# Performance work log

Hardware: AMD Instinct MI355X
Metric: run time of the kernel (lower is better)

The kernel has to match this reference:

```python
import jax, jax.numpy as jnp
import numpy as np

TAU = 2.0       # init_tau
VTH = 1.0       # v_threshold
VRESET = 0.0    # v_reset (hard reset)
ALPHA = 2.0     # ATan surrogate width
H = 8           # num_heads
W = 20          # attention_window
TIME_STEP = 2   # config.time_step -> global_scale uses 1000 // time_step


@jax.custom_vjp
def spike(x):
    return (x >= 0.0).astype(x.dtype)

def _spike_fwd(x):
    return (x >= 0.0).astype(x.dtype), x

def _spike_bwd(x, g):
    # ATan surrogate gradient (spikingjelly default)
    sg = (ALPHA / 2.0) / (1.0 + (jnp.pi / 2.0 * ALPHA * x) ** 2)
    return (g * sg,)

spike.defvjp(_spike_fwd, _spike_bwd)


def lif(x_seq):
    """Multi-step LIF, decay_input=False, hard reset. x_seq: [T, ...] -> spikes [T, ...]."""
    def step(v, x):
        h = v - (v - VRESET) / TAU + x          # neuronal charge (decay_input=False)
        s = spike(h - VTH)
        v_new = s * VRESET + (1.0 - s) * h      # hard reset
        return v_new, s
    _, s_seq = jax.lax.scan(step, jnp.zeros_like(x_seq[0]), x_seq)
    return s_seq


def bn(x, gamma, beta, eps=1e-5):
    # BatchNorm1d step_mode='m': stats over (T, B) per channel (training-mode stats)
    mean = x.mean(axis=(0, 1))
    var = x.var(axis=(0, 1))
    return (x - mean) * jax.lax.rsqrt(var + eps) * gamma + beta


def _shift(a, o):
    # a: [B, H, T, D]; out[..., t, :] = a[..., t + o, :], zero outside -> local band
    if o == 0:
        return a
    B_, H_, T_, D_ = a.shape
    z = jnp.zeros((B_, H_, abs(o), D_), a.dtype)
    if o > 0:
        return jnp.concatenate([a[:, :, o:, :], z], axis=2)
    return jnp.concatenate([z, a[:, :, :o, :]], axis=2)


def _forward(x, wq, wk, wv, w_mattn, w_proj, w_dw, w_pw, bn_gamma, bn_beta):
    T, B, C = x.shape
    D = C // H
    local_scale = 1.0 / np.sqrt(D * (2 * W + 1)).astype(np.float32)
    global_scale = 1.0 / np.sqrt(D * (1000 // TIME_STEP)).astype(np.float32)

    # spiking QKV: pointwise conv (kernel 1) + BN + LIF
    q = lif(bn(jnp.einsum('tbc,dc->tbd', x, wq), bn_gamma[0], bn_beta[0]))
    k = lif(bn(jnp.einsum('tbc,dc->tbd', x, wk), bn_gamma[1], bn_beta[1]))
    v = lif(bn(jnp.einsum('tbc,dc->tbd', x, wv), bn_gamma[2], bn_beta[2]))

    heads = lambda a: a.reshape(T, B, H, D).transpose(1, 2, 0, 3)   # [B,H,T,D]
    unheads = lambda a: a.transpose(2, 0, 1, 3).reshape(T, B, C)    # [T,B,C]
    qh, kh, vh = heads(q), heads(k), heads(v)

    # global spiking self-attention (no softmax): (Q K^T) V * global_scale
    attn = jnp.einsum('bhtd,bhsd->bhts', qh, kh)
    g_spk = lif(unheads(jnp.einsum('bhts,bhsd->bhtd', attn, vh) * global_scale))

    # local sliding-window attention over offsets [-W, W] (banded, no [T,T] matrix)
    out_l = jnp.zeros_like(vh)
    for o in range(-W, W + 1):
        s = jnp.einsum('bhtd,bhtd->bht', qh, _shift(kh, o))
        out_l = out_l + s[..., None] * _shift(vh, o)
    l_spk = lif(unheads(out_l * local_scale))

    # depthwise temporal conv branch on V: v_dw -> LIF -> v_pw (1x1 over heads)
    dw = jax.lax.conv_general_dilated(
        vh, w_dw, window_strides=(1, 1), padding=((4, 4), (0, 0)),
        dimension_numbers=('NCHW', 'OIHW', 'NCHW'), feature_group_count=H)
    dw_spk_h = heads(lif(unheads(dw)))
    dw_out = unheads(jnp.einsum('bhtd,gh->bgtd', dw_spk_h, w_pw))

    # merge branches, then mattn conv+BN+LIF and proj conv+BN+LIF
    y0 = lif(g_spk + l_spk + dw_out)
    y1 = lif(bn(jnp.einsum('tbc,dc->tbd', y0, w_mattn), bn_gamma[3], bn_beta[3]))
    out = lif(bn(jnp.einsum('tbc,dc->tbd', y1, w_proj), bn_gamma[4], bn_beta[4]))
    return out


def setup_inputs() -> dict:
    key = jax.random.key(0)
    ks = jax.random.split(key, 10)
    T, B, C = 500, 8, 512
    sc = 0.03
    x = jax.random.normal(ks[0], (T, B, C), jnp.float32)
    wq = jax.random.normal(ks[1], (C, C), jnp.float32) * sc
    wk = jax.random.normal(ks[2], (C, C), jnp.float32) * sc
    wv = jax.random.normal(ks[3], (C, C), jnp.float32) * sc
    w_mattn = jax.random.normal(ks[4], (C, C), jnp.float32) * sc
    w_proj = jax.random.normal(ks[5], (C, C), jnp.float32) * sc
    w_dw = jax.random.normal(ks[6], (H, 1, 9, 1), jnp.float32) * 0.3   # depthwise (9,1)
    w_pw = jax.random.normal(ks[7], (H, H), jnp.float32) * 0.3         # 1x1 over heads
    bn_gamma = jax.random.uniform(ks[8], (5, C), jnp.float32) + 0.5
    bn_beta = jax.random.normal(ks[9], (5, C), jnp.float32) * 0.1
    return {'x': x, 'wq': wq, 'wk': wk, 'wv': wv, 'w_mattn': w_mattn,
            'w_proj': w_proj, 'w_dw': w_dw, 'w_pw': w_pw,
            'bn_gamma': bn_gamma, 'bn_beta': bn_beta}


def reference(x, wq, wk, wv, w_mattn, w_proj, w_dw, w_pw, bn_gamma, bn_beta):
    return _forward(x, wq, wk, wv, w_mattn, w_proj, w_dw, w_pw, bn_gamma, bn_beta)
```

## Files before the change

### kernel.cpp

```cpp
#include <hip/hip_runtime.h>
#include <cmath>

#define TT 500
#define NTOT 2048000
#define WW 20

typedef _Float16 f16x8 __attribute__((ext_vector_type(8)));
typedef _Float16 f16x4 __attribute__((ext_vector_type(4)));
typedef float f32x4 __attribute__((ext_vector_type(4)));

#define C1SC 4.8828125e-4f
#define C2SC 2.384185791015625e-7f

__global__ __launch_bounds__(256) void prep_split_k(
    const float* __restrict__ x, const float* __restrict__ wq,
    const float* __restrict__ wk, const float* __restrict__ wv,
    const float* __restrict__ wm, const float* __restrict__ wp,
    _Float16* __restrict__ X0, _Float16* __restrict__ X1, _Float16* __restrict__ X2,
    _Float16* __restrict__ Q0, _Float16* __restrict__ Q1, _Float16* __restrict__ Q2,
    _Float16* __restrict__ M0, _Float16* __restrict__ M1, _Float16* __restrict__ M2,
    _Float16* __restrict__ P0, _Float16* __restrict__ P1, _Float16* __restrict__ P2)
{
    int gid = blockIdx.x * 256 + threadIdx.x;
    const float* src;
    _Float16 *d0, *d1, *d2;
    size_t si, di;
    if (gid < 512000) {
        src = x; d0 = X0; d1 = X1; d2 = X2; si = di = (size_t)gid * 4;
    } else if (gid < 708608) {
        int g = gid - 512000;
        int s3 = g >> 16;
        src = (s3 == 0) ? wq : ((s3 == 1) ? wk : wv);
        d0 = Q0; d1 = Q1; d2 = Q2;
        si = (size_t)(g & 65535) * 4;
        di = (size_t)g * 4;
    } else if (gid < 774144) {
        int g = gid - 708608;
        src = wm; d0 = M0; d1 = M1; d2 = M2; si = di = (size_t)g * 4;
    } else {
        int g = gid - 774144;
        src = wp; d0 = P0; d1 = P1; d2 = P2; si = di = (size_t)g * 4;
    }
    float4 v = *(const float4*)(src + si);
    float f[4] = {v.x, v.y, v.z, v.w};
    f16x4 a, b, c;
#pragma unroll
    for (int i = 0; i < 4; ++i) {
        _Float16 h0 = (_Float16)f[i];
        float r1 = f[i] - (float)h0;
        _Float16 h1 = (_Float16)(r1 * 2048.0f);
        float r2 = r1 - (float)h1 * C1SC;
        _Float16 h2 = (_Float16)(r2 * 4194304.0f);
        a[i] = h0; b[i] = h1; c[i] = h2;
    }
    *(f16x4*)(d0 + di) = a;
    *(f16x4*)(d1 + di) = b;
    *(f16x4*)(d2 + di) = c;
}

__global__ __launch_bounds__(256) void gemm_f16s3_k(
    const _Float16* __restrict__ X0, const _Float16* __restrict__ X1,
    const _Float16* __restrict__ X2,
    const _Float16* __restrict__ B0g, const _Float16* __restrict__ B1g,
    const _Float16* __restrict__ B2g,
    float* __restrict__ out, float* __restrict__ colpart, int M)
{
    __shared__ __align__(16) _Float16 sA[23040];
    int tid = threadIdx.x;
    int bid = blockIdx.x;
    int xcd = bid & 7;
    int j = bid >> 3;
    int mblk = (xcd << 3) | (j & 7);
    int nblk = j >> 3;
    int mBase = mblk * 64;
    int nBase = nblk * 128;
    int arow = tid >> 2;
    int ak = (tid & 3) * 8;
    int wv = tid >> 6;
    int lane = tid & 63;
    int wr = wv >> 1, wc = wv & 1;
    int lg = lane >> 4, l16 = lane & 15;

    f32x4 acc0[2][4] = {}, acc1[2][4] = {}, acc2[2][4] = {};
    f16x8 pa0, pa1, pa2, pb0[2], pb1[2], pb2[2];
    f16x8 hz = {};

    auto loadT = [&](int kt) {
        int m = mBase + arow;
        if (m < M) {
            pa0 = *(const f16x8*)(X0 + (size_t)m * 512 + kt + ak);
            pa1 = *(const f16x8*)(X1 + (size_t)m * 512 + kt + ak);
            pa2 = *(const f16x8*)(X2 + (size_t)m * 512 + kt + ak);
        } else { pa0 = hz; pa1 = hz; pa2 = hz; }
#pragma unroll
        for (int l = 0; l < 2; ++l) {
            int r = nBase + arow + l * 64;
            pb0[l] = *(const f16x8*)(B0g + (size_t)r * 512 + kt + ak);
            pb1[l] = *(const f16x8*)(B1g + (size_t)r * 512 + kt + ak);
            pb2[l] = *(const f16x8*)(B2g + (size_t)r * 512 + kt + ak);
        }
    };
    loadT(0);
    for (int kt = 0; kt < 512; kt += 32) {
        __syncthreads();
        {
            int ao = arow * 40 + ak;
            *(f16x8*)&sA[ao] = pa0;
            *(f16x8*)&sA[2560 + ao] = pa1;
            *(f16x8*)&sA[5120 + ao] = pa2;
#pragma unroll
            for (int l = 0; l < 2; ++l) {
                int bo = (arow + l * 64) * 40 + ak;
                *(f16x8*)&sA[7680 + bo] = pb0[l];
                *(f16x8*)&sA[12800 + bo] = pb1[l];
                *(f16x8*)&sA[17920 + bo] = pb2[l];
            }
        }
        __syncthreads();
        if (kt + 32 < 512) loadT(kt + 32);
        f16x8 a0f[2], a1f[2], a2f[2];
#pragma unroll
        for (int i = 0; i < 2; ++i) {
            int off = (wr * 32 + i * 16 + l16) * 40 + lg * 8;
            a0f[i] = *(const f16x8*)&sA[off];
            a1f[i] = *(const f16x8*)&sA[2560 + off];
            a2f[i] = *(const f16x8*)&sA[5120 + off];
        }
#pragma unroll
        for (int jj = 0; jj < 4; ++jj) {
            int boff = (wc * 64 + jj * 16 + l16) * 40 + lg * 8;
            f16x8 b0f = *(const f16x8*)&sA[7680 + boff];
            f16x8 b1f = *(const f16x8*)&sA[12800 + boff];
            f16x8 b2f = *(const f16x8*)&sA[17920 + boff];
#pragma unroll
            for (int i = 0; i < 2; ++i) {
                acc0[i][jj] = __builtin_amdgcn_mfma_f32_16x16x32_f16(a0f[i], b0f, acc0[i][jj], 0, 0, 0);
                acc1[i][jj] = __builtin_amdgcn_mfma_f32_16x16x32_f16(a0f[i], b1f, acc1[i][jj], 0, 0, 0);
                acc1[i][jj] = __builtin_amdgcn_mfma_f32_16x16x32_f16(a1f[i], b0f, acc1[i][jj], 0, 0, 0);
                acc2[i][jj] = __builtin_amdgcn_mfma_f32_16x16x32_f16(a1f[i], b1f, acc2[i][jj], 0, 0, 0);
                acc2[i][jj] = __builtin_amdgcn_mfma_f32_16x16x32_f16(a0f[i], b2f, acc2[i][jj], 0, 0, 0);
                acc2[i][jj] = __builtin_amdgcn_mfma_f32_16x16x32_f16(a2f[i], b0f, acc2[i][jj], 0, 0, 0);
            }
        }
    }
#pragma unroll
    for (int i = 0; i < 2; ++i)
#pragma unroll
        for (int jj = 0; jj < 4; ++jj)
#pragma unroll
            for (int r = 0; r < 4; ++r)
                acc0[i][jj][r] = fmaf(C2SC, acc2[i][jj][r],
                                      fmaf(C1SC, acc1[i][jj][r], acc0[i][jj][r]));
    __syncthreads();
    float* red = (float*)sA;
#pragma unroll
    for (int jj = 0; jj < 4; ++jj) {
        float s = 0.f, q = 0.f;
#pragma unroll
        for (int i = 0; i < 2; ++i)
#pragma unroll
            for (int r = 0; r < 4; ++r) { float v = acc0[i][jj][r]; s += v; q = fmaf(v, v, q); }
        s += __shfl_xor(s, 16, 64); s += __shfl_xor(s, 32, 64);
        q += __shfl_xor(q, 16, 64); q += __shfl_xor(q, 32, 64);
        if (lane < 16) {
            int col = wc * 64 + jj * 16 + lane;
            red[(wr * 128 + col) * 2 + 0] = s;
            red[(wr * 128 + col) * 2 + 1] = q;
        }
    }
    __syncthreads();
    if (tid < 128) {
        float ss = red[tid * 2 + 0] + red[(128 + tid) * 2 + 0];
        float qq = red[tid * 2 + 1] + red[(128 + tid) * 2 + 1];
        colpart[((size_t)mblk * 1536 + nBase + tid) * 2 + 0] = ss;
        colpart[((size_t)mblk * 1536 + nBase + tid) * 2 + 1] = qq;
    }
    int wsel = nBase >> 9;
    int col0 = nBase & 511;
    float* outp = out + (size_t)wsel * NTOT;
#pragma unroll
    for (int i = 0; i < 2; ++i) {
        int m0 = mBase + wr * 32 + i * 16 + lg * 4;
#pragma unroll
        for (int jj = 0; jj < 4; ++jj) {
            int cc = col0 + wc * 64 + jj * 16 + l16;
#pragma unroll
            for (int r = 0; r < 4; ++r) {
                int m = m0 + r;
                if (m < M) outp[(size_t)m * 512 + cc] = acc0[i][jj][r];
            }
        }
    }
}

__global__ __launch_bounds__(256) void gemm_hs3_k(
    const _Float16* __restrict__ Ah,
    const _Float16* __restrict__ B0g, const _Float16* __restrict__ B1g,
    const _Float16* __restrict__ B2g,
    float* __restrict__ out, float* __restrict__ colpart, int M)
{
    __shared__ __align__(16) _Float16 sA[10240];
    int tid = threadIdx.x;
    int bid = blockIdx.x;
    int xcd = bid & 7;
    int j = bid >> 3;
    int mblk = (xcd << 3) | (j & 7);
    int nblk = j >> 3;
    int mBase = mblk * 64;
    int col0 = nblk * 64;
    int arow = tid >> 2;
    int ak = (tid & 3) * 8;
    int wv = tid >> 6;
    int lane = tid & 63;
    int wr = wv >> 1, wc = wv & 1;
    int lg = lane >> 4, l16 = lane & 15;

    f32x4 acc0[2][2] = {}, acc1[2][2] = {}, acc2[2][2] = {};
    f16x8 pa, pb0, pb1, pb2;
    f16x8 hz = {};

    auto loadT = [&](int kt) {
        int m = mBase + arow;
        pa = (m < M) ? *(const f16x8*)(Ah + (size_t)m * 512 + kt + ak) : hz;
        int r = col0 + arow;
        pb0 = *(const f16x8*)(B0g + (size_t)r * 512 + kt + ak);
        pb1 = *(const f16x8*)(B1g + (size_t)r * 512 + kt + ak);
        pb2 = *(const f16x8*)(B2g + (size_t)r * 512 + kt + ak);
    };
    loadT(0);
    for (int kt = 0; kt < 512; kt += 32) {
        __syncthreads();
        {
            int ao = arow * 40 + ak;
            *(f16x8*)&sA[ao] = pa;
            *(f16x8*)&sA[2560 + ao] = pb0;
            *(f16x8*)&sA[5120 + ao] = pb1;
            *(f16x8*)&sA[7680 + ao] = pb2;
        }
        __syncthreads();
        if (kt + 32 < 512) loadT(kt + 32);
        f16x8 af[2];
#pragma unroll
        for (int i = 0; i < 2; ++i)
            af[i] = *(const f16x8*)&sA[(wr * 32 + i * 16 + l16) * 40 + lg * 8];
#pragma unroll
        for (int jj = 0; jj < 2; ++jj) {
            int boff = (wc * 32 + jj * 16 + l16) * 40 + lg * 8;
            f16x8 b0f = *(const f16x8*)&sA[2560 + boff];
            f16x8 b1f = *(const f16x8*)&sA[5120 + boff];
            f16x8 b2f = *(const f16x8*)&sA[7680 + boff];
#pragma unroll
            for (int i = 0; i < 2; ++i) {
                acc0[i][jj] = __builtin_amdgcn_mfma_f32_16x16x32_f16(af[i], b0f, acc0[i][jj], 0, 0, 0);
                acc1[i][jj] = __builtin_amdgcn_mfma_f32_16x16x32_f16(af[i], b1f, acc1[i][jj], 0, 0, 0);
                acc2[i][jj] = __builtin_amdgcn_mfma_f32_16x16x32_f16(af[i], b2f, acc2[i][jj], 0, 0, 0);
            }
        }
    }
#pragma unroll
    for (int i = 0; i < 2; ++i)
#pragma unroll
        for (int jj = 0; jj < 2; ++jj)
#pragma unroll
            for (int r = 0; r < 4; ++r)
                acc0[i][jj][r] = fmaf(C2SC, acc2[i][jj][r],
                                      fmaf(C1SC, acc1[i][jj][r], acc0[i][jj][r]));
    __syncthreads();
    float* red = (float*)sA;
#pragma unroll
    for (int jj = 0; jj < 2; ++jj) {
        float s = 0.f, q = 0.f;
#pragma unroll
        for (int i = 0; i < 2; ++i)
#pragma unroll
            for (int r = 0; r < 4; ++r) { float v = acc0[i][jj][r]; s += v; q = fmaf(v, v, q); }
        s += __shfl_xor(s, 16, 64); s += __shfl_xor(s, 32, 64);
        q += __shfl_xor(q, 16, 64); q += __shfl_xor(q, 32, 64);
        if (lane < 16) {
            int col = wc * 32 + jj * 16 + lane;
            red[(wr * 64 + col) * 2 + 0] = s;
            red[(wr * 64 + col) * 2 + 1] = q;
        }
    }
    __syncthreads();
    if (tid < 64) {
        float ss = red[tid * 2 + 0] + red[(64 + tid) * 2 + 0];
        float qq = red[tid * 2 + 1] + red[(64 + tid) * 2 + 1];
        colpart[((size_t)mblk * 512 + col0 + tid) * 2 + 0] = ss;
        colpart[((size_t)mblk * 512 + col0 + tid) * 2 + 1] = qq;
    }
#pragma unroll
    for (int i = 0; i < 2; ++i) {
        int m0 = mBase + wr * 32 + i * 16 + lg * 4;
#pragma unroll
        for (int jj = 0; jj < 2; ++jj) {
            int cc = col0 + wc * 32 + jj * 16 + l16;
#pragma unroll
            for (int r = 0; r < 4; ++r) {
                int m = m0 + r;
                if (m < M) out[(size_t)m * 512 + cc] = acc0[i][jj][r];
            }
        }
    }
}

__global__ __launch_bounds__(256) void lif_seg_k(
    const float* __restrict__ pre, const float* __restrict__ colpart, int CT, int chunks,
    const float* __restrict__ gamma, const float* __restrict__ beta,
    float* __restrict__ outF, unsigned char* __restrict__ outB,
    _Float16* __restrict__ outH, int segLen, int warm)
{
    int gid = blockIdx.x * 256 + threadIdx.x;
    int tensor = gid >> 12;
    int bc = gid & 4095;
    int ch = (tensor << 9) | (bc & 511);
    double s = 0.0, s2 = 0.0;
    for (int k = 0; k < chunks; ++k) {
        s  += (double)colpart[((size_t)k * CT + ch) * 2 + 0];
        s2 += (double)colpart[((size_t)k * CT + ch) * 2 + 1];
    }
    double mean = s / 4000.0;
    double var = s2 / 4000.0 - mean * mean;
    double scd = (double)gamma[ch] / sqrt(var + 1e-5);
    float sc = (float)scd;
    float sh = (float)((double)beta[ch] - mean * scd);
    const float* q0 = pre + (size_t)tensor * NTOT + bc;
    float* oF = outF ? outF + (size_t)tensor * NTOT + bc : nullptr;
    unsigned char* oB = outB ? outB + (size_t)tensor * NTOT + bc : nullptr;
    _Float16* oH = outH ? outH + (size_t)tensor * NTOT + bc : nullptr;
    int t0 = blockIdx.y * segLen;
    int twarm = (t0 - warm > 0) ? (t0 - warm) : 0;
    int tend = (t0 + segLen < TT) ? (t0 + segLen) : TT;
    float v = 0.f;
    float b0[8];
#pragma unroll
    for (int j = 0; j < 8; ++j) {
        int tt = twarm + j;
        b0[j] = (tt < tend) ? q0[(size_t)tt * 4096] : 0.f;
    }
    for (int t = twarm; t < tend; t += 8) {
        float n0[8];
#pragma unroll
        for (int j = 0; j < 8; ++j) {
            int tt = t + 8 + j;
            n0[j] = (tt < tend) ? q0[(size_t)tt * 4096] : 0.f;
        }
#pragma unroll
        for (int j = 0; j < 8; ++j) {
            int tc = t + j;
            if (tc >= tend) break;
            float bnx = fmaf(b0[j], sc, sh);
            float h = fmaf(0.5f, v, bnx);
            float sp = (h >= 1.f) ? 1.f : 0.f;
            v = (h >= 1.f) ? 0.f : h;
            if (tc >= t0) {
                if (oB)      oB[(size_t)tc * 4096] = (unsigned char)sp;
                else if (oH) oH[(size_t)tc * 4096] = (_Float16)sp;
                else         oF[(size_t)tc * 4096] = sp;
            }
        }
#pragma unroll
        for (int j = 0; j < 8; ++j) b0[j] = n0[j];
    }
}

__global__ __launch_bounds__(256) void ktv_part_k(
    const unsigned char* __restrict__ kspk, const unsigned char* __restrict__ vspk,
    float* __restrict__ part)
{
    __shared__ __align__(16) float kb[16][64], vb[16][64];
    int bh = blockIdx.x;
    int seg = blockIdx.y;
    int t0p = seg * 125, t1p = t0p + 125;
    int b = bh >> 3, h = bh & 7;
    int tid = threadIdx.x;
    int d1b = (tid >> 4) * 4, d2b = (tid & 15) * 4;
    size_t cb = (size_t)b * 512 + h * 64;
    int sRow = tid >> 4;
    int sD = (tid & 15) * 4;
    float acc[4][4] = {};
    uchar4 pk, pv;
    auto preload = [&](int tt) {
        int t = tt + sRow;
        if (t < t1p) {
            pk = *(const uchar4*)(kspk + (size_t)t * 4096 + cb + sD);
            pv = *(const uchar4*)(vspk + (size_t)t * 4096 + cb + sD);
        } else {
            pk = make_uchar4(0, 0, 0, 0); pv = make_uchar4(0, 0, 0, 0);
        }
    };
    preload(t0p);
    for (int tt = t0p; tt < t1p; tt += 16) {
        __syncthreads();
        kb[sRow][sD + 0] = (float)pk.x; kb[sRow][sD + 1] = (float)pk.y;
        kb[sRow][sD + 2] = (float)pk.z; kb[sRow][sD + 3] = (float)pk.w;
        vb[sRow][sD + 0] = (float)pv.x; vb[sRow][sD + 1] = (float)pv.y;
        vb[sRow][sD + 2] = (float)pv.z; vb[sRow][sD + 3] = (float)pv.w;
        __syncthreads();
        preload(tt + 16);
#pragma unroll
        for (int tl = 0; tl < 16; ++tl) {
            float4 k4 = *(const float4*)&kb[tl][d1b];
            float4 v4 = *(const float4*)&vb[tl][d2b];
            float ka[4] = {k4.x, k4.y, k4.z, k4.w};
            float va[4] = {v4.x, v4.y, v4.z, v4.w};
#pragma unroll
            for (int i = 0; i < 4; ++i)
#pragma unroll
                for (int j = 0; j < 4; ++j)
                    acc[i][j] = fmaf(ka[i], va[j], acc[i][j]);
        }
    }
    size_t ob = ((size_t)seg * 64 + bh) * 4096;
#pragma unroll
    for (int i = 0; i < 4; ++i)
        *(float4*)(part + ob + (size_t)(d1b + i) * 64 + d2b) =
            make_float4(acc[i][0], acc[i][1], acc[i][2], acc[i][3]);
}

__global__ __launch_bounds__(256) void ktv_reduce_k(
    const float* __restrict__ part, float* __restrict__ ktv)
{
    int i4 = (blockIdx.x * 256 + threadIdx.x) * 4;
    float4 a = *(const float4*)(part + i4);
    float4 b = *(const float4*)(part + 262144 + i4);
    float4 c = *(const float4*)(part + 2 * 262144 + i4);
    float4 d = *(const float4*)(part + 3 * 262144 + i4);
    *(float4*)(ktv + i4) = make_float4(((a.x + b.x) + c.x) + d.x,
                                       ((a.y + b.y) + c.y) + d.y,
                                       ((a.z + b.z) + c.z) + d.z,
                                       ((a.w + b.w) + c.w) + d.w);
}

__global__ __launch_bounds__(256) void gapply_t_k(
    const unsigned char* __restrict__ sq, const float* __restrict__ ktv,
    float* __restrict__ gpre, float gscale)
{
    __shared__ float qs[10][512];
    int tid = threadIdx.x;
    int t0 = blockIdx.x * 10;
    int b = blockIdx.y;
    for (int i = tid; i < 1280; i += 256) {
        int t = i >> 7;
        int c4 = (i & 127) * 4;
        uchar4 u = *(const uchar4*)(sq + (size_t)(t0 + t) * 4096 + b * 512 + c4);
        qs[t][c4 + 0] = (float)u.x; qs[t][c4 + 1] = (float)u.y;
        qs[t][c4 + 2] = (float)u.z; qs[t][c4 + 3] = (float)u.w;
    }
    __syncthreads();
#pragma unroll
    for (int half = 0; half < 2; ++half) {
        int c = tid + half * 256;
        int h = c >> 6, dcol = c & 63;
        const float* kt = ktv + ((size_t)(b * 8 + h) * 64) * 64 + dcol;
        float acc[10] = {};
        for (int d1 = 0; d1 < 64; ++d1) {
            float kv = kt[(size_t)d1 * 64];
#pragma unroll
            for (int t = 0; t < 10; ++t)
                acc[t] = fmaf(qs[t][h * 64 + d1], kv, acc[t]);
        }
#pragma unroll
        for (int t = 0; t < 10; ++t)
            gpre[(size_t)(t0 + t) * 4096 + b * 512 + c] = acc[t] * gscale;
    }
}

__global__ __launch_bounds__(256) void local_k(
    const unsigned char* __restrict__ qspk, const unsigned char* __restrict__ kspk,
    const unsigned char* __restrict__ vspk, float* __restrict__ lpre, float lscale)
{
    __shared__ __align__(16) float qs[32][68];
    __shared__ __align__(16) float ks[72][68];
    __shared__ __align__(16) float vs[72][68];
    __shared__ float sm[32][72];
    int t0 = blockIdx.x * 32;
    int bh = blockIdx.y;
    int b = bh >> 3, h = bh & 7;
    int tid = threadIdx.x;
    size_t cb = (size_t)b * 512 + h * 64;

    for (int i = tid; i < 512; i += 256) {
        int r = i >> 4, d4 = (i & 15) * 4;
        int t = t0 + r;
        if (t < TT) {
            uchar4 u = *(const uchar4*)(qspk + (size_t)t * 4096 + cb + d4);
            qs[r][d4 + 0] = (float)u.x; qs[r][d4 + 1] = (float)u.y;
            qs[r][d4 + 2] = (float)u.z; qs[r][d4 + 3] = (float)u.w;
        } else {
            qs[r][d4 + 0] = 0.f; qs[r][d4 + 1] = 0.f; qs[r][d4 + 2] = 0.f; qs[r][d4 + 3] = 0.f;
        }
    }
    for (int i = tid; i < 1152; i += 256) {
        int r = i >> 4, d4 = (i & 15) * 4;
        int u_ = t0 - WW + r;
        if (u_ >= 0 && u_ < TT) {
            uchar4 uk = *(const uchar4*)(kspk + (size_t)u_ * 4096 + cb + d4);
            uchar4 uv = *(const uchar4*)(vspk + (size_t)u_ * 4096 + cb + d4);
            ks[r][d4 + 0] = (float)uk.x; ks[r][d4 + 1] = (float)uk.y;
            ks[r][d4 + 2] = (float)uk.z; ks[r][d4 + 3] = (float)uk.w;
            vs[r][d4 + 0] = (float)uv.x; vs[r][d4 + 1] = (float)uv.y;
            vs[r][d4 + 2] = (float)uv.z; vs[r][d4 + 3] = (float)uv.w;
        } else {
            ks[r][d4 + 0] = 0.f; ks[r][d4 + 1] = 0.f; ks[r][d4 + 2] = 0.f; ks[r][d4 + 3] = 0.f;
            vs[r][d4 + 0] = 0.f; vs[r][d4 + 1] = 0.f; vs[r][d4 + 2] = 0.f; vs[r][d4 + 3] = 0.f;
        }
    }
    __syncthreads();

    int tA = tid >> 3;
    int ug = tid & 7;
    float4 qreg[16];
#pragma unroll
    for (int i = 0; i < 16; ++i) qreg[i] = *(const float4*)&qs[tA][i * 4];
#pragma unroll
    for (int ui = 0; ui < 9; ++ui) {
        int u = ug + ui * 8;
        float acc = 0.f;
#pragma unroll
        for (int i = 0; i < 16; ++i) {
            float4 k4 = *(const float4*)&ks[u][i * 4];
            acc = fmaf(qreg[i].x, k4.x, acc);
            acc = fmaf(qreg[i].y, k4.y, acc);
            acc = fmaf(qreg[i].z, k4.z, acc);
            acc = fmaf(qreg[i].w, k4.w, acc);
        }
        sm[tA][u] = acc;
    }
    __syncthreads();

#pragma unroll
    for (int oi = 0; oi < 2; ++oi) {
        int idx = tid + oi * 256;
        int t = idx >> 4;
        int dg = (idx & 15) * 4;
        float4 acc = make_float4(0.f, 0.f, 0.f, 0.f);
        for (int o = 0; o < 41; ++o) {
            int u = t + o;
            float s = sm[t][u];
            float4 v4 = *(const float4*)&vs[u][dg];
            acc.x = fmaf(s, v4.x, acc.x);
            acc.y = fmaf(s, v4.y, acc.y);
            acc.z = fmaf(s, v4.z, acc.z);
            acc.w = fmaf(s, v4.w, acc.w);
        }
        int tg = t0 + t;
        if (tg < TT) {
            acc.x *= lscale; acc.y *= lscale; acc.z *= lscale; acc.w *= lscale;
            *(float4*)(lpre + (size_t)tg * 4096 + cb + dg) = acc;
        }
    }
}

__global__ __launch_bounds__(256) void branch_y0_k(
    const float* __restrict__ gpre, const float* __restrict__ lpre,
    const unsigned char* __restrict__ sv, const float* __restrict__ wdw,
    const float* __restrict__ wpw, _Float16* __restrict__ sy0,
    int segLen, int warm)
{
    int tid = threadIdx.x;
    int wave = tid >> 6, lane = tid & 63;
    int gw = blockIdx.x * 4 + wave;
    int b = gw >> 3, dg = gw & 7;
    int h = lane >> 3, dl = lane & 7;
    int c = h * 64 + dg * 8 + dl;
    int base = b * 512 + c;
    float w9[9];
#pragma unroll
    for (int j = 0; j < 9; ++j) w9[j] = wdw[h * 9 + j];
    float w8[8];
#pragma unroll
    for (int j = 0; j < 8; ++j) w8[j] = wpw[h * 8 + j];
    int t0 = blockIdx.y * segLen;
    int twarm = (t0 - warm > 0) ? (t0 - warm) : 0;
    int tend = (t0 + segLen < TT) ? (t0 + segLen) : TT;
    float vg = 0.f, vl = 0.f, vd = 0.f, vy = 0.f;
    float win[12];
#pragma unroll
    for (int i = 0; i < 12; ++i) {
        int tt = twarm - 4 + i;
        win[i] = (tt >= 0 && tt < TT) ? (float)sv[(size_t)tt * 4096 + base] : 0.f;
    }
    float pg[4], pl[4], pv[4];
    auto pref = [&](int t) {
#pragma unroll
        for (int j = 0; j < 4; ++j) {
            int tt = t + j;
            bool in = tt < tend;
            pg[j] = in ? gpre[(size_t)tt * 4096 + base] : 0.f;
            pl[j] = in ? lpre[(size_t)tt * 4096 + base] : 0.f;
            int tv = t + 8 + j;
            pv[j] = (tv < TT) ? (float)sv[(size_t)tv * 4096 + base] : 0.f;
        }
    };
    pref(twarm);
    for (int t = twarm; t < tend; t += 4) {
        float cg[4], cl[4], cv[4];
#pragma unroll
        for (int j = 0; j < 4; ++j) { cg[j] = pg[j]; cl[j] = pl[j]; cv[j] = pv[j]; }
        pref(t + 4);
#pragma unroll
        for (int j = 0; j < 4; ++j) {
            int tc = t + j;
            if (tc >= tend) break;
            float x = 0.f;
#pragma unroll
            for (int q = 0; q < 9; ++q) x = fmaf(w9[q], win[j + q], x);
            float hd = fmaf(0.5f, vd, x);
            float sd = (hd >= 1.f) ? 1.f : 0.f;
            vd = (hd >= 1.f) ? 0.f : hd;
            float hg = fmaf(0.5f, vg, cg[j]);
            float sg = (hg >= 1.f) ? 1.f : 0.f;
            vg = (hg >= 1.f) ? 0.f : hg;
            float hl = fmaf(0.5f, vl, cl[j]);
            float sl = (hl >= 1.f) ? 1.f : 0.f;
            vl = (hl >= 1.f) ? 0.f : hl;
            float mix = 0.f;
#pragma unroll
            for (int h2 = 0; h2 < 8; ++h2)
                mix = fmaf(w8[h2], __shfl(sd, h2 * 8 + dl, 64), mix);
            float xy = (sg + sl) + mix;
            float hy = fmaf(0.5f, vy, xy);
            float sy = (hy >= 1.f) ? 1.f : 0.f;
            vy = (hy >= 1.f) ? 0.f : hy;
            if (tc >= t0) sy0[(size_t)tc * 4096 + base] = (_Float16)sy;
        }
#pragma unroll
        for (int i = 0; i < 8; ++i) win[i] = win[i + 4];
#pragma unroll
        for (int i = 0; i < 4; ++i) win[8 + i] = cv[i];
    }
}

extern "C" void kernel_launch(void* const* d_in, const int* in_sizes, int n_in,
                              void* d_out, int out_size, void* d_ws, size_t ws_size,
                              hipStream_t stream)
{
    const float* x       = (const float*)d_in[0];
    const float* wq      = (const float*)d_in[1];
    const float* wk      = (const float*)d_in[2];
    const float* wv      = (const float*)d_in[3];
    const float* w_mattn = (const float*)d_in[4];
    const float* w_proj  = (const float*)d_in[5];
    const float* w_dw    = (const float*)d_in[6];
    const float* w_pw    = (const float*)d_in[7];
    const float* bn_g    = (const float*)d_in[8];
    const float* bn_b    = (const float*)d_in[9];
    float* out = (float*)d_out;
    float* ws = (float*)d_ws;

    float gs32 = (float)std::sqrt((double)(64 * 500));
    float gscale = (float)(1.0 / (double)gs32);
    float ls32 = (float)std::sqrt((double)(64 * 41));
    float lscale = (float)(1.0 / (double)ls32);
    const int M = TT * 8;

    float* S0 = ws;
    float* S1 = ws + (size_t)NTOT;
    float* S2 = ws + 2 * (size_t)NTOT;
    float* part4   = ws + 3 * (size_t)NTOT;
    float* ktvBuf  = part4 + 4 * 262144;
    float* colpart = ktvBuf + 262144;
    unsigned char* spk = (unsigned char*)(colpart + 196608);
    unsigned char* sq  = spk;
    unsigned char* sk  = spk + (size_t)NTOT;
    unsigned char* sv  = spk + 2 * (size_t)NTOT;
    _Float16* sy0h = (_Float16*)(spk + 3 * (size_t)NTOT);
    _Float16* sy1h = (_Float16*)spk;
    _Float16* X0 = (_Float16*)spk;
    _Float16* X1 = X0 + (size_t)NTOT;
    _Float16* X2 = X1 + (size_t)NTOT;
    _Float16* Wm0 = (_Float16*)(spk + 6 * (size_t)NTOT);
    _Float16* Wm1 = Wm0 + 262144;
    _Float16* Wm2 = Wm1 + 262144;
    _Float16* Wp0 = Wm2 + 262144;
    _Float16* Wp1 = Wp0 + 262144;
    _Float16* Wp2 = Wp1 + 262144;
    _Float16* Wq0 = (_Float16*)part4;
    _Float16* Wq1 = Wq0 + 786432;
    _Float16* Wq2 = Wq1 + 786432;

    prep_split_k<<<3280, 256, 0, stream>>>(x, wq, wk, wv, w_mattn, w_proj,
                                           X0, X1, X2, Wq0, Wq1, Wq2,
                                           Wm0, Wm1, Wm2, Wp0, Wp1, Wp2);
    gemm_f16s3_k<<<768, 256, 0, stream>>>(X0, X1, X2, Wq0, Wq1, Wq2, S0, colpart, M);
    lif_seg_k<<<dim3(48, 10), 256, 0, stream>>>(S0, colpart, 1536, 64, bn_g, bn_b,
                                                nullptr, sq, nullptr, 50, 64);
    ktv_part_k<<<dim3(64, 4), 256, 0, stream>>>(sk, sv, part4);
    ktv_reduce_k<<<256, 256, 0, stream>>>(part4, ktvBuf);
    gapply_t_k<<<dim3(50, 8), 256, 0, stream>>>(sq, ktvBuf, S0, gscale);
    local_k<<<dim3(16, 64), 256, 0, stream>>>(sq, sk, sv, S1, lscale);
    branch_y0_k<<<dim3(16, 20), 256, 0, stream>>>(S0, S1, sv, w_dw, w_pw, sy0h, 25, 64);
    gemm_hs3_k<<<512, 256, 0, stream>>>(sy0h, Wm0, Wm1, Wm2, S2, colpart, M);
    lif_seg_k<<<dim3(16, 20), 256, 0, stream>>>(S2, colpart, 512, 64, bn_g + 1536,
                                                bn_b + 1536, nullptr, nullptr, sy1h, 25, 64);
    gemm_hs3_k<<<512, 256, 0, stream>>>(sy1h, Wp0, Wp1, Wp2, S0, colpart, M);
    lif_seg_k<<<dim3(16, 20), 256, 0, stream>>>(S0, colpart, 512, 64, bn_g + 2048,
                                                bn_b + 2048, out, nullptr, nullptr, 25, 64);

    (void)in_sizes; (void)n_in; (void)out_size; (void)ws_size;
}
```

Before: 351.9 us.

## Use direct global-to-LDS loads with XOR swizzle in split-fp16 GEMMs

Both split-precision GEMM kernels now copy A/B tiles straight into LDS with global_load_lds instead of staging through registers, and use an XOR-swizzled 32-wide layout in place of the padded 40-wide one. This is meant to cut VGPR pressure and the register-to-LDS store instructions, and to lower LDS use so occupancy can rise. The register prefetch of the next tile is gone, so global loads no longer overlap with MFMA work inside a block. Out-of-range rows now read row 0 rather than zeros, so the column statistics mask those rows explicitly.

```diff
diff --git a/kernel.cpp b/kernel.cpp
--- a/kernel.cpp
+++ b/kernel.cpp
@@ -11,6 +11,12 @@
 
 #define C1SC 4.8828125e-4f
 #define C2SC 2.384185791015625e-7f
+
+__device__ __forceinline__ void gload16(const _Float16* g, _Float16* l) {
+    __builtin_amdgcn_global_load_lds(
+        (const __attribute__((address_space(1))) unsigned int*)g,
+        (__attribute__((address_space(3))) unsigned int*)l, 16, 0, 0);
+}
 
 __global__ __launch_bounds__(256) void prep_split_k(
     const float* __restrict__ x, const float* __restrict__ wq,
@@ -65,7 +71,7 @@
     const _Float16* __restrict__ B2g,
     float* __restrict__ out, float* __restrict__ colpart, int M)
 {
-    __shared__ __align__(16) _Float16 sA[23040];
+    __shared__ __align__(16) _Float16 sA[18432];
     int tid = threadIdx.x;
     int bid = blockIdx.x;
     int xcd = bid & 7;
@@ -74,64 +80,66 @@
     int nblk = j >> 3;
     int mBase = mblk * 64;
     int nBase = nblk * 128;
-    int arow = tid >> 2;
-    int ak = (tid & 3) * 8;
     int wv = tid >> 6;
     int lane = tid & 63;
     int wr = wv >> 1, wc = wv & 1;
     int lg = lane >> 4, l16 = lane & 15;
 
+    int subrow = lane >> 2;
+    int s4 = lane & 3;
+    int rA = (wv << 4) + subrow;
+    int sl8 = (s4 ^ ((rA >> 1) & 3)) * 8;
+    int mA = mBase + rA; if (mA >= M) mA = 0;
+    const _Float16* gA0 = X0 + (size_t)mA * 512 + sl8;
+    const _Float16* gA1 = X1 + (size_t)mA * 512 + sl8;
+    const _Float16* gA2 = X2 + (size_t)mA * 512 + sl8;
+    const _Float16* gB00 = B0g + (size_t)(nBase + rA) * 512 + sl8;
+    const _Float16* gB01 = B0g + (size_t)(nBase + 64 + rA) * 512 + sl8;
+    const _Float16* gB10 = B1g + (size_t)(nBase + rA) * 512 + sl8;
+    const _Float16* gB11 = B1g + (size_t)(nBase + 64 + rA) * 512 + sl8;
+    const _Float16* gB20 = B2g + (size_t)(nBase + rA) * 512 + sl8;
+    const _Float16* gB21 = B2g + (size_t)(nBase + 64 + rA) * 512 + sl8;
+    int wb = wv << 9;
+    _Float16* lA0 = sA + wb;
+    _Float16* lA1 = sA + 2048 + wb;
+    _Float16* lA2 = sA + 4096 + wb;
+    _Float16* lB00 = sA + 6144 + wb;
+    _Float16* lB01 = sA + 8192 + wb;
+    _Float16* lB10 = sA + 10240 + wb;
+    _Float16* lB11 = sA + 12288 + wb;
+    _Float16* lB20 = sA + 14336 + wb;
+    _Float16* lB21 = sA + 16384 + wb;
+
+    int sd = (lg ^ ((l16 >> 1) & 3)) * 8;
+
     f32x4 acc0[2][4] = {}, acc1[2][4] = {}, acc2[2][4] = {};
-    f16x8 pa0, pa1, pa2, pb0[2], pb1[2], pb2[2];
-    f16x8 hz = {};
-
-    auto loadT = [&](int kt) {
-        int m = mBase + arow;
-        if (m < M) {
-            pa0 = *(const f16x8*)(X0 + (size_t)m * 512 + kt + ak);
-            pa1 = *(const f16x8*)(X1 + (size_t)m * 512 + kt + ak);
-            pa2 = *(const f16x8*)(X2 + (size_t)m * 512 + kt + ak);
-        } else { pa0 = hz; pa1 = hz; pa2 = hz; }
-#pragma unroll
-        for (int l = 0; l < 2; ++l) {
-            int r = nBase + arow + l * 64;
-            pb0[l] = *(const f16x8*)(B0g + (size_t)r * 512 + kt + ak);
-            pb1[l] = *(const f16x8*)(B1g + (size_t)r * 512 + kt + ak);
-            pb2[l] = *(const f16x8*)(B2g + (size_t)r * 512 + kt + ak);
-        }
-    };
-    loadT(0);
+
     for (int kt = 0; kt < 512; kt += 32) {
         __syncthreads();
-        {
-            int ao = arow * 40 + ak;
-            *(f16x8*)&sA[ao] = pa0;
-            *(f16x8*)&sA[2560 + ao] = pa1;
-            *(f16x8*)&sA[5120 + ao] = pa2;
-#pragma unroll
-            for (int l = 0; l < 2; ++l) {
-                int bo = (arow + l * 64) * 40 + ak;
-                *(f16x8*)&sA[7680 + bo] = pb0[l];
-                *(f16x8*)&sA[12800 + bo] = pb1[l];
-                *(f16x8*)&sA[17920 + bo] = pb2[l];
-            }
-        }
+        gload16(gA0 + kt, lA0);
+        gload16(gA1 + kt, lA1);
+        gload16(gA2 + kt, lA2);
+        gload16(gB00 + kt, lB00);
+        gload16(gB01 + kt, lB01);
+        gload16(gB10 + kt, lB10);
+        gload16(gB11 + kt, lB11);
+        gload16(gB20 + kt, lB20);
+        gload16(gB21 + kt, lB21);
         __syncthreads();
-        if (kt + 32 < 512) loadT(kt + 32);
         f16x8 a0f[2], a1f[2], a2f[2];
 #pragma unroll
         for (int i = 0; i < 2; ++i) {
-            int off = (wr * 32 + i * 16 + l16) * 40 + lg * 8;
+            int off = (wr * 32 + i * 16 + l16) * 32 + sd;
             a0f[i] = *(const f16x8*)&sA[off];
-            a1f[i] = *(const f16x8*)&sA[2560 + off];
-            a2f[i] = *(const f16x8*)&sA[5120 + off];
+            a1f[i] = *(const f16x8*)&sA[2048 + off];
+            a2f[i] = *(const f16x8*)&sA[4096 + off];
         }
 #pragma unroll
         for (int jj = 0; jj < 4; ++jj) {
-            int boff = (wc * 64 + jj * 16 + l16) * 40 + lg * 8;
-            f16x8 b0f = *(const f16x8*)&sA[7680 + boff];
-            f16x8 b1f = *(const f16x8*)&sA[12800 + boff];
-            f16x8 b2f = *(const f16x8*)&sA[17920 + boff];
+            int boff = 6144 + (wc * 64 + jj * 16 + l16) * 32 + sd;
+            f16x8 b0f = *(const f16x8*)&sA[boff];
+            f16x8 b1f = *(const f16x8*)&sA[4096 + boff];
+            f16x8 b2f = *(const f16x8*)&sA[8192 + boff];
 #pragma unroll
             for (int i = 0; i < 2; ++i) {
                 acc0[i][jj] = __builtin_amdgcn_mfma_f32_16x16x32_f16(a0f[i], b0f, acc0[i][jj], 0, 0, 0);
@@ -159,7 +167,11 @@
 #pragma unroll
         for (int i = 0; i < 2; ++i)
 #pragma unroll
-            for (int r = 0; r < 4; ++r) { float v = acc0[i][jj][r]; s += v; q = fmaf(v, v, q); }
+            for (int r = 0; r < 4; ++r) {
+                int mrow = mBase + wr * 32 + i * 16 + lg * 4 + r;
+                float v = (mrow < M) ? acc0[i][jj][r] : 0.f;
+                s += v; q = fmaf(v, v, q);
+            }
         s += __shfl_xor(s, 16, 64); s += __shfl_xor(s, 32, 64);
         q += __shfl_xor(q, 16, 64); q += __shfl_xor(q, 32, 64);
         if (lane < 16) {
@@ -199,7 +211,7 @@
     const _Float16* __restrict__ B2g,
     float* __restrict__ out, float* __restrict__ colpart, int M)
 {
-    __shared__ __align__(16) _Float16 sA[10240];
+    __shared__ __align__(16) _Float16 sH[8192];
     int tid = threadIdx.x;
     int bid = blockIdx.x;
     int xcd = bid & 7;
@@ -208,47 +220,47 @@
     int nblk = j >> 3;
     int mBase = mblk * 64;
     int col0 = nblk * 64;
-    int arow = tid >> 2;
-    int ak = (tid & 3) * 8;
     int wv = tid >> 6;
     int lane = tid & 63;
     int wr = wv >> 1, wc = wv & 1;
     int lg = lane >> 4, l16 = lane & 15;
 
+    int subrow = lane >> 2;
+    int s4 = lane & 3;
+    int rA = (wv << 4) + subrow;
+    int sl8 = (s4 ^ ((rA >> 1) & 3)) * 8;
+    int mA = mBase + rA; if (mA >= M) mA = 0;
+    const _Float16* gA  = Ah  + (size_t)mA * 512 + sl8;
+    const _Float16* gB0 = B0g + (size_t)(col0 + rA) * 512 + sl8;
+    const _Float16* gB1 = B1g + (size_t)(col0 + rA) * 512 + sl8;
+    const _Float16* gB2 = B2g + (size_t)(col0 + rA) * 512 + sl8;
+    int wb = wv << 9;
+    _Float16* lA  = sH + wb;
+    _Float16* lB0 = sH + 2048 + wb;
+    _Float16* lB1 = sH + 4096 + wb;
+    _Float16* lB2 = sH + 6144 + wb;
+
+    int sd = (lg ^ ((l16 >> 1) & 3)) * 8;
+
     f32x4 acc0[2][2] = {}, acc1[2][2] = {}, acc2[2][2] = {};
-    f16x8 pa, pb0, pb1, pb2;
-    f16x8 hz = {};
-
-    auto loadT = [&](int kt) {
-        int m = mBase + arow;
-        pa = (m < M) ? *(const f16x8*)(Ah + (size_t)m * 512 + kt + ak) : hz;
-        int r = col0 + arow;
-        pb0 = *(const f16x8*)(B0g + (size_t)r * 512 + kt + ak);
-        pb1 = *(const f16x8*)(B1g + (size_t)r * 512 + kt + ak);
-        pb2 = *(const f16x8*)(B2g + (size_t)r * 512 + kt + ak);
-    };
-    loadT(0);
+
     for (int kt = 0; kt < 512; kt += 32) {
         __syncthreads();
-        {
-            int ao = arow * 40 + ak;
-            *(f16x8*)&sA[ao] = pa;
-            *(f16x8*)&sA[2560 + ao] = pb0;
-            *(f16x8*)&sA[5120 + ao] = pb1;
-            *(f16x8*)&sA[7680 + ao] = pb2;
-        }
+        gload16(gA + kt, lA);
+        gload16(gB0 + kt, lB0);
+        gload16(gB1 + kt, lB1);
+        gload16(gB2 + kt, lB2);
         __syncthreads();
-        if (kt + 32 < 512) loadT(kt + 32);
         f16x8 af[2];
 #pragma unroll
         for (int i = 0; i < 2; ++i)
-            af[i] = *(const f16x8*)&sA[(wr * 32 + i * 16 + l16) * 40 + lg * 8];
+            af[i] = *(const f16x8*)&sH[(wr * 32 + i * 16 + l16) * 32 + sd];
 #pragma unroll
         for (int jj = 0; jj < 2; ++jj) {
-            int boff = (wc * 32 + jj * 16 + l16) * 40 + lg * 8;
-            f16x8 b0f = *(const f16x8*)&sA[2560 + boff];
-            f16x8 b1f = *(const f16x8*)&sA[5120 + boff];
-            f16x8 b2f = *(const f16x8*)&sA[7680 + boff];
+            int boff = 2048 + (wc * 32 + jj * 16 + l16) * 32 + sd;
+            f16x8 b0f = *(const f16x8*)&sH[boff];
+            f16x8 b1f = *(const f16x8*)&sH[2048 + boff];
+            f16x8 b2f = *(const f16x8*)&sH[4096 + boff];
 #pragma unroll
             for (int i = 0; i < 2; ++i) {
                 acc0[i][jj] = __builtin_amdgcn_mfma_f32_16x16x32_f16(af[i], b0f, acc0[i][jj], 0, 0, 0);
@@ -266,14 +278,18 @@
                 acc0[i][jj][r] = fmaf(C2SC, acc2[i][jj][r],
                                       fmaf(C1SC, acc1[i][jj][r], acc0[i][jj][r]));
     __syncthreads();
-    float* red = (float*)sA;
+    float* red = (float*)sH;
 #pragma unroll
     for (int jj = 0; jj < 2; ++jj) {
         float s = 0.f, q = 0.f;
 #pragma unroll
         for (int i = 0; i < 2; ++i)
 #pragma unroll
-            for (int r = 0; r < 4; ++r) { float v = acc0[i][jj][r]; s += v; q = fmaf(v, v, q); }
+            for (int r = 0; r < 4; ++r) {
+                int mrow = mBase + wr * 32 + i * 16 + lg * 4 + r;
+                float v = (mrow < M) ? acc0[i][jj][r] : 0.f;
+                s += v; q = fmaf(v, v, q);
+            }
         s += __shfl_xor(s, 16, 64); s += __shfl_xor(s, 32, 64);
         q += __shfl_xor(q, 16, 64); q += __shfl_xor(q, 32, 64);
         if (lane < 16) {
```

After: 341.6 us. 1.03x faster.
